# Kernel optimization log

Measured on AMD Instinct MI355X. Metric: run time of the kernel, lower is better.

The kernel has to match this reference:

```python
import jax, jax.numpy as jnp
import numpy as np

CONFIDENCE = 0.1
EPS = 1e-3  # keras BatchNormalization default epsilon
B, H, W, C = 4, 64, 64, 256


def setup_inputs() -> dict:
    key = jax.random.key(0)
    ks = jax.random.split(key, 6)
    return {
        "x": jax.random.normal(ks[0], (B, H, W, C), jnp.float32),
        "ca_gamma": jnp.ones((C,), jnp.float32),
        "ca_beta": jnp.zeros((C,), jnp.float32),
        "ca_mean": jnp.zeros((C,), jnp.float32),
        "ca_var": jnp.ones((C,), jnp.float32),
        "wq": jax.random.normal(ks[1], (C, C), jnp.float32) * 0.05,
        "wk": jax.random.normal(ks[2], (C, C), jnp.float32) * 0.05,
        "wv": jax.random.normal(ks[3], (C, C), jnp.float32) * 0.05,
        "wp": jax.random.normal(ks[4], (C, C), jnp.float32) * 0.05,
        "bn_gamma": jnp.ones((C,), jnp.float32),
        "bn_beta": jnp.zeros((C,), jnp.float32),
        "bn_mean": jnp.zeros((C,), jnp.float32),
        "bn_var": jnp.ones((C,), jnp.float32),
        "w_qkv": jax.random.normal(ks[5], (C, 3), jnp.float32) * 0.05,
    }


def _bn(x, g, b, m, v):
    # keras BatchNormalization, inference mode
    return (x - m) * jax.lax.rsqrt(v + EPS) * g + b


def reference(x, ca_gamma, ca_beta, ca_mean, ca_var, wq, wk, wv, wp,
              bn_gamma, bn_beta, bn_mean, bn_var, w_qkv):
    b, h, w, c = x.shape
    # ---- ChannelAttention (TRACER Channel_Tracer; dropout = identity at inference) ----
    gap = x.mean(axis=(1, 2))                         # [B, C] global average pool
    gn = _bn(gap, ca_gamma, ca_beta, ca_mean, ca_var)  # [B, C]
    q = gn @ wq                                        # 1x1 conv on 1x1 map == matmul
    k = gn @ wk
    v = gn @ wv
    logits = q[:, :, None] * k[:, None, :]             # [B, C, C], head_dim = 1
    score = jax.nn.softmax(logits, axis=-1)
    att = jnp.einsum('bij,bj->bi', score, v)           # [B, C]
    cmask = jax.nn.sigmoid(att @ wp)                   # [B, C] channel mask (alpha)
    ca_out = x * cmask[:, None, None, :] + x           # residual channel re-weighting
    # ---- UnionAttention spatial part ----
    co = _bn(ca_out, bn_gamma, bn_beta, bn_mean, bn_var)
    thr = jnp.percentile(cmask, CONFIDENCE * 100.0, axis=-1,
                         keepdims=True, method='linear')  # [B, 1]
    pmask = jnp.where(cmask > thr, cmask, 0.0)          # percentile masking
    co = co * pmask[:, None, None, :]
    qkv = jnp.einsum('bhwc,cf->bhwf', co, w_qkv)        # [B, H, W, 3] fused q/k/v 1x1 conv
    n = h * w
    qs = qkv[..., 0].reshape(b, n)                      # [B, N], head_dim = 1
    ks_ = qkv[..., 1].reshape(b, n)
    vs = qkv[..., 2].reshape(b, n)
    sl = qs[:, :, None] * ks_[:, None, :]               # [B, N, N] scores (outer product)
    sw = jax.nn.softmax(sl, axis=-1)
    sa = jnp.einsum('bij,bj->bi', sw, vs)               # [B, N]
    return qkv[..., 2:3] + sa.reshape(b, h, w, 1)       # v + attention, [B, H, W, 1]
```

## Files before the change

### kernel.cpp

```cpp
#include <hip/hip_runtime.h>

#define EPS 1e-3f

#define OFF_PGAP   0
#define OFF_A      65536
#define OFF_BIAS   66560
#define OFF_QS     66576
#define OFF_KS     82960
#define OFF_VS     99344

__global__ __launch_bounds__(256) void k_gap(const float* __restrict__ x,
                                             float* __restrict__ pgap) {
    int blk = blockIdx.x;
    int t = threadIdx.x;
    const float* xp = x + (size_t)blk * (64 * 256) + t;
    float s = 0.f;
    #pragma unroll 16
    for (int p = 0; p < 64; ++p) s += xp[(size_t)p * 256];
    pgap[blk * 256 + t] = s;
}

__global__ __launch_bounds__(512) void k_mid(
    const float* __restrict__ pgap,
    const float* __restrict__ cag, const float* __restrict__ cab,
    const float* __restrict__ cam, const float* __restrict__ cav,
    const float* __restrict__ wq, const float* __restrict__ wk,
    const float* __restrict__ wv, const float* __restrict__ wp,
    const float* __restrict__ bng, const float* __restrict__ bnb,
    const float* __restrict__ bnm, const float* __restrict__ bnv,
    const float* __restrict__ wqkv,
    float* __restrict__ Aout, float* __restrict__ biasOut)
{
    __shared__ float gn[256];
    __shared__ float sq[256], sk[256], sv[256], att[256], cm[256], Bc[256];
    __shared__ float red[6144];
    __shared__ float swqkv[768];
    __shared__ float t25, t26, thr;

    int b = blockIdx.x;
    int t = threadIdx.x;
    int cg = t & 63;
    int rg = t >> 6;
    int c4 = cg * 4;

    if (t < 384) {
        swqkv[t] = wqkv[t];
        swqkv[t + 384] = wqkv[t + 384];
    }

    {
        const float* pg = pgap + (size_t)(b * 64 + rg * 8) * 256 + c4;
        float4 s = make_float4(0.f, 0.f, 0.f, 0.f);
        #pragma unroll
        for (int u = 0; u < 8; ++u) {
            float4 v = *(const float4*)(pg + (size_t)u * 256);
            s.x += v.x; s.y += v.y; s.z += v.z; s.w += v.w;
        }
        *(float4*)(red + rg * 256 + c4) = s;
    }
    __syncthreads();
    if (t < 256) {
        float g = 0.f;
        #pragma unroll
        for (int r = 0; r < 8; ++r) g += red[r * 256 + t];
        g *= (1.0f / 4096.0f);
        float sc = cag[t] * rsqrtf(cav[t] + EPS);
        gn[t] = g * sc + (cab[t] - cam[t] * sc);
    }
    __syncthreads();

    {
        int rbase = rg * 32;
        float4 aq = make_float4(0.f, 0.f, 0.f, 0.f);
        float4 ak = aq, av = aq;
        const float* wqp = wq + (size_t)rbase * 256 + c4;
        const float* wkp = wk + (size_t)rbase * 256 + c4;
        const float* wvp = wv + (size_t)rbase * 256 + c4;
        #pragma unroll 8
        for (int i = 0; i < 32; ++i) {
            float g = gn[rbase + i];
            float4 w = *(const float4*)(wqp + (size_t)i * 256);
            aq.x = fmaf(g, w.x, aq.x); aq.y = fmaf(g, w.y, aq.y);
            aq.z = fmaf(g, w.z, aq.z); aq.w = fmaf(g, w.w, aq.w);
        }
        #pragma unroll 8
        for (int i = 0; i < 32; ++i) {
            float g = gn[rbase + i];
            float4 w = *(const float4*)(wkp + (size_t)i * 256);
            ak.x = fmaf(g, w.x, ak.x); ak.y = fmaf(g, w.y, ak.y);
            ak.z = fmaf(g, w.z, ak.z); ak.w = fmaf(g, w.w, ak.w);
        }
        #pragma unroll 8
        for (int i = 0; i < 32; ++i) {
            float g = gn[rbase + i];
            float4 w = *(const float4*)(wvp + (size_t)i * 256);
            av.x = fmaf(g, w.x, av.x); av.y = fmaf(g, w.y, av.y);
            av.z = fmaf(g, w.z, av.z); av.w = fmaf(g, w.w, av.w);
        }
        *(float4*)(red + (0 * 8 + rg) * 256 + c4) = aq;
        *(float4*)(red + (1 * 8 + rg) * 256 + c4) = ak;
        *(float4*)(red + (2 * 8 + rg) * 256 + c4) = av;
    }
    __syncthreads();
    {
        int m = t >> 8, c = t & 255;
        float s = 0.f;
        #pragma unroll
        for (int r = 0; r < 8; ++r) s += red[(m * 8 + r) * 256 + c];
        if (m == 0) sq[c] = s; else sk[c] = s;
        if (t < 256) {
            float s2 = 0.f;
            #pragma unroll
            for (int r = 0; r < 8; ++r) s2 += red[(2 * 8 + r) * 256 + t];
            sv[t] = s2;
        }
    }
    __syncthreads();

    {
        int h = t >> 8, c = t & 255;
        float a = sq[c];
        int jb = h * 128;
        float mx = -1e30f;
        #pragma unroll 8
        for (int j = 0; j < 128; ++j) mx = fmaxf(mx, a * sk[jb + j]);
        float den = 0.f, num = 0.f;
        #pragma unroll 4
        for (int j = 0; j < 128; ++j) {
            float e = __expf(a * sk[jb + j] - mx);
            den += e; num = fmaf(e, sv[jb + j], num);
        }
        red[h * 256 + c] = mx;
        red[512 + h * 256 + c] = den;
        red[1024 + h * 256 + c] = num;
    }
    __syncthreads();
    if (t < 256) {
        float m0 = red[t], m1 = red[256 + t];
        float M = fmaxf(m0, m1);
        float s0 = __expf(m0 - M), s1 = __expf(m1 - M);
        float den = red[512 + t] * s0 + red[768 + t] * s1;
        float num = red[1024 + t] * s0 + red[1280 + t] * s1;
        att[t] = num / den;
    }
    __syncthreads();

    {
        int rbase = rg * 32;
        float4 ac = make_float4(0.f, 0.f, 0.f, 0.f);
        const float* wpp = wp + (size_t)rbase * 256 + c4;
        #pragma unroll 8
        for (int i = 0; i < 32; ++i) {
            float g = att[rbase + i];
            float4 w = *(const float4*)(wpp + (size_t)i * 256);
            ac.x = fmaf(g, w.x, ac.x); ac.y = fmaf(g, w.y, ac.y);
            ac.z = fmaf(g, w.z, ac.z); ac.w = fmaf(g, w.w, ac.w);
        }
        *(float4*)(red + rg * 256 + c4) = ac;
    }
    __syncthreads();
    if (t < 256) {
        float ac = 0.f;
        #pragma unroll
        for (int r = 0; r < 8; ++r) ac += red[r * 256 + t];
        cm[t] = 1.0f / (1.0f + __expf(-ac));
    }
    __syncthreads();

    if (t < 256) {
        float my = cm[t];
        int rank = 0;
        for (int j = 0; j < 256; ++j) {
            float o = cm[j];
            rank += (o < my) ? 1 : ((o == my && j < t) ? 1 : 0);
        }
        if (rank == 25) t25 = my;
        if (rank == 26) t26 = my;
    }
    __syncthreads();
    if (t == 0) thr = t25 + 0.5f * (t26 - t25);
    __syncthreads();

    if (t < 256) {
        float s2 = bng[t] * rsqrtf(bnv[t] + EPS);
        float o2 = bnb[t] - bnm[t] * s2;
        float cc = cm[t];
        float pm = (cc > thr) ? cc : 0.f;
        Aout[b * 256 + t] = (1.f + cc) * s2 * pm;
        Bc[t] = o2 * pm;
    }
    __syncthreads();
    if (t < 3) {
        float s3 = 0.f;
        for (int ch = 0; ch < 256; ++ch) s3 = fmaf(Bc[ch], swqkv[ch * 3 + t], s3);
        biasOut[b * 3 + t] = s3;
    }
}

__global__ __launch_bounds__(256) void k_qkv(
    const float* __restrict__ x, const float* __restrict__ A,
    const float* __restrict__ wqkv, const float* __restrict__ bias,
    float* __restrict__ qs, float* __restrict__ ks, float* __restrict__ vs)
{
    int lane = threadIdx.x & 63;
    int wid = (blockIdx.x * 256 + threadIdx.x) >> 6;
    float4 wA = *(const float4*)(wqkv + 12 * lane);
    float4 wB = *(const float4*)(wqkv + 12 * lane + 4);
    float4 wC = *(const float4*)(wqkv + 12 * lane + 8);
    float w00 = wA.x, w01 = wA.y, w02 = wA.z;
    float w10 = wA.w, w11 = wB.x, w12 = wB.y;
    float w20 = wB.z, w21 = wB.w, w22 = wC.x;
    float w30 = wC.y, w31 = wC.z, w32 = wC.w;
    #pragma unroll
    for (int b = 0; b < 4; ++b) {
        int pix = b * 4096 + wid;
        float4 xv = *(const float4*)(x + (size_t)pix * 256 + 4 * lane);
        float4 A4 = *(const float4*)(A + b * 256 + 4 * lane);
        float t0 = xv.x * A4.x, t1 = xv.y * A4.y;
        float t2 = xv.z * A4.z, t3 = xv.w * A4.w;
        float q = t0 * w00 + t1 * w10 + t2 * w20 + t3 * w30;
        float k = t0 * w01 + t1 * w11 + t2 * w21 + t3 * w31;
        float v = t0 * w02 + t1 * w12 + t2 * w22 + t3 * w32;
        #pragma unroll
        for (int m = 1; m < 64; m <<= 1) {
            q += __shfl_xor(q, m, 64);
            k += __shfl_xor(k, m, 64);
            v += __shfl_xor(v, m, 64);
        }
        if (lane == 0) {
            qs[pix] = q + bias[b * 3 + 0];
            ks[pix] = k + bias[b * 3 + 1];
            vs[pix] = v + bias[b * 3 + 2];
        }
    }
}

__global__ __launch_bounds__(512) void k_attn2(
    const float* __restrict__ qs, const float* __restrict__ ks, const float* __restrict__ vs,
    float* __restrict__ out)
{
    __shared__ float4 skv[2048];
    __shared__ float pden[8][64], pnum[8][64];
    __shared__ float rmax[8], rmin[8];
    int blk = blockIdx.x;
    int b = blk >> 6, ic = blk & 63;
    int t = threadIdx.x;
    int lane = t & 63, sub = t >> 6;
    int base = b * 4096;

    const float4* k4 = (const float4*)(ks + base);
    const float4* v4 = (const float4*)(vs + base);
    float kmx = -1e30f, kmn = 1e30f;
    #pragma unroll
    for (int u = 0; u < 2; ++u) {
        int i = t + u * 512;
        float4 kk = k4[i], vv = v4[i];
        skv[i * 2]     = make_float4(kk.x, vv.x, kk.y, vv.y);
        skv[i * 2 + 1] = make_float4(kk.z, vv.z, kk.w, vv.w);
        kmx = fmaxf(kmx, fmaxf(fmaxf(kk.x, kk.y), fmaxf(kk.z, kk.w)));
        kmn = fminf(kmn, fminf(fminf(kk.x, kk.y), fminf(kk.z, kk.w)));
    }
    #pragma unroll
    for (int m2 = 1; m2 < 64; m2 <<= 1) {
        kmx = fmaxf(kmx, __shfl_xor(kmx, m2, 64));
        kmn = fminf(kmn, __shfl_xor(kmn, m2, 64));
    }
    if (lane == 0) { rmax[sub] = kmx; rmin[sub] = kmn; }
    __syncthreads();
    float mx = rmax[0], mn = rmin[0];
    #pragma unroll
    for (int s = 1; s < 8; ++s) { mx = fmaxf(mx, rmax[s]); mn = fminf(mn, rmin[s]); }

    int row = ic * 64 + lane;
    float a = qs[base + row];
    float m = (a >= 0.f) ? a * mx : a * mn;
    float den0 = 0.f, num0 = 0.f, den1 = 0.f, num1 = 0.f;
    const float4* sp = skv + sub * 256;
    #pragma unroll 4
    for (int j = 0; j < 256; ++j) {
        float4 kv = sp[j];
        float e0 = __expf(fmaf(a, kv.x, -m));
        float e1 = __expf(fmaf(a, kv.z, -m));
        den0 += e0; num0 = fmaf(e0, kv.y, num0);
        den1 += e1; num1 = fmaf(e1, kv.w, num1);
    }
    pden[sub][lane] = den0 + den1;
    pnum[sub][lane] = num0 + num1;
    __syncthreads();
    if (t < 64) {
        float den = 0.f, num = 0.f;
        #pragma unroll
        for (int s = 0; s < 8; ++s) { den += pden[s][t]; num += pnum[s][t]; }
        int r = ic * 64 + t;
        float vrow = (r & 1) ? skv[r >> 1].w : skv[r >> 1].y;
        out[base + r] = vrow + num / den;
    }
}

extern "C" void kernel_launch(void* const* d_in, const int* in_sizes, int n_in,
                              void* d_out, int out_size, void* d_ws, size_t ws_size,
                              hipStream_t stream) {
    const float* x    = (const float*)d_in[0];
    const float* cag  = (const float*)d_in[1];
    const float* cab  = (const float*)d_in[2];
    const float* cam  = (const float*)d_in[3];
    const float* cav  = (const float*)d_in[4];
    const float* wq   = (const float*)d_in[5];
    const float* wk   = (const float*)d_in[6];
    const float* wv   = (const float*)d_in[7];
    const float* wp   = (const float*)d_in[8];
    const float* bng  = (const float*)d_in[9];
    const float* bnb  = (const float*)d_in[10];
    const float* bnm  = (const float*)d_in[11];
    const float* bnv  = (const float*)d_in[12];
    const float* wqkv = (const float*)d_in[13];

    float* ws   = (float*)d_ws;
    float* pgap = ws + OFF_PGAP;
    float* A    = ws + OFF_A;
    float* bias = ws + OFF_BIAS;
    float* qs   = ws + OFF_QS;
    float* ks   = ws + OFF_KS;
    float* vs   = ws + OFF_VS;

    k_gap<<<dim3(256), dim3(256), 0, stream>>>(x, pgap);
    k_mid<<<dim3(4), dim3(512), 0, stream>>>(pgap, cag, cab, cam, cav, wq, wk, wv, wp,
                                             bng, bnb, bnm, bnv, wqkv, A, bias);
    k_qkv<<<dim3(1024), dim3(256), 0, stream>>>(x, A, wqkv, bias, qs, ks, vs);
    k_attn2<<<dim3(256), dim3(512), 0, stream>>>(qs, ks, vs, (float*)d_out);
}
```

Measured before the change: 140.9 us.

## Split channel-attention GEMVs into a parallel kernel and prefetch weights in GAP

Moves the q/k/v GEMV out of the 4-block k_mid kernel into a new 96-block k_qkvmat kernel. Each block handles 8 weight rows for all batches and writes partial sums, which k_mid then reduces. k_gap now uses float4 loads with an in-block reduction, and it also touches the wq/wk/wv/wp weights so they are pulled into cache before the serial stages. The aim is to cut the latency of the low-parallelism middle stage. The cost is an extra kernel launch and a partial-sum buffer round trip.

```diff
diff --git a/kernel.cpp b/kernel.cpp
--- a/kernel.cpp
+++ b/kernel.cpp
@@ -3,37 +3,109 @@
 #define EPS 1e-3f
 
 #define OFF_PGAP   0
-#define OFF_A      65536
-#define OFF_BIAS   66560
-#define OFF_QS     66576
-#define OFF_KS     82960
-#define OFF_VS     99344
+#define OFF_PART   65536
+#define OFF_A      163840
+#define OFF_BIAS   164864
+#define OFF_QS     164880
+#define OFF_KS     181264
+#define OFF_VS     197648
 
 __global__ __launch_bounds__(256) void k_gap(const float* __restrict__ x,
+                                             const float* __restrict__ wq,
+                                             const float* __restrict__ wk,
+                                             const float* __restrict__ wv,
+                                             const float* __restrict__ wp,
                                              float* __restrict__ pgap) {
+    __shared__ float4 red[256];
     int blk = blockIdx.x;
     int t = threadIdx.x;
-    const float* xp = x + (size_t)blk * (64 * 256) + t;
-    float s = 0.f;
-    #pragma unroll 16
-    for (int p = 0; p < 64; ++p) s += xp[(size_t)p * 256];
-    pgap[blk * 256 + t] = s;
-}
-
-__global__ __launch_bounds__(512) void k_mid(
+
+    const float* wmat = (blk < 64) ? wq : (blk < 128) ? wk : (blk < 192) ? wv : wp;
+    float4 wv4 = *(const float4*)(wmat + (size_t)(blk & 63) * 1024 + 4 * t);
+
+    int cg = t & 63;
+    int pg = t >> 6;
+    const float* xp = x + ((size_t)blk * 64 + pg * 16) * 256 + 4 * cg;
+    float4 s = make_float4(0.f, 0.f, 0.f, 0.f);
+    #pragma unroll
+    for (int u = 0; u < 16; ++u) {
+        float4 v = *(const float4*)(xp + (size_t)u * 256);
+        s.x += v.x; s.y += v.y; s.z += v.z; s.w += v.w;
+    }
+    red[pg * 64 + cg] = s;
+    asm volatile("" :: "v"(wv4.x), "v"(wv4.y), "v"(wv4.z), "v"(wv4.w));
+    __syncthreads();
+    if (t < 64) {
+        float4 a = red[t], b4 = red[64 + t], c4 = red[128 + t], d4 = red[192 + t];
+        float4 o = make_float4(a.x + b4.x + c4.x + d4.x,
+                               a.y + b4.y + c4.y + d4.y,
+                               a.z + b4.z + c4.z + d4.z,
+                               a.w + b4.w + c4.w + d4.w);
+        *(float4*)(pgap + blk * 256 + 4 * t) = o;
+    }
+}
+
+__global__ __launch_bounds__(256) void k_qkvmat(
     const float* __restrict__ pgap,
     const float* __restrict__ cag, const float* __restrict__ cab,
     const float* __restrict__ cam, const float* __restrict__ cav,
     const float* __restrict__ wq, const float* __restrict__ wk,
-    const float* __restrict__ wv, const float* __restrict__ wp,
+    const float* __restrict__ wv,
+    float* __restrict__ part)
+{
+    __shared__ float gpart[4][8][4];
+    __shared__ float gn_s[4][8];
+    int blk = blockIdx.x;
+    int m = blk >> 5;
+    int g = blk & 31;
+    int r0 = g * 8;
+    int t = threadIdx.x;
+    const float* W = (m == 0) ? wq : (m == 1) ? wk : wv;
+
+    if (t < 128) {
+        int b = t >> 5, row = (t >> 2) & 7, p = t & 3;
+        const float* pgp = pgap + ((size_t)(b * 64 + p * 16)) * 256 + r0 + row;
+        float s = 0.f;
+        #pragma unroll
+        for (int ch = 0; ch < 16; ++ch) s += pgp[(size_t)ch * 256];
+        gpart[b][row][p] = s;
+    }
+    __syncthreads();
+    if (t < 32) {
+        int b = t >> 3, row = t & 7;
+        float gsum = gpart[b][row][0] + gpart[b][row][1]
+                   + gpart[b][row][2] + gpart[b][row][3];
+        float gv = gsum * (1.0f / 4096.0f);
+        int c = r0 + row;
+        float sc = cag[c] * rsqrtf(cav[c] + EPS);
+        gn_s[b][row] = gv * sc + (cab[c] - cam[c] * sc);
+    }
+    __syncthreads();
+
+    float a0 = 0.f, a1 = 0.f, a2 = 0.f, a3 = 0.f;
+    const float* wp_ = W + (size_t)r0 * 256 + t;
+    #pragma unroll
+    for (int row = 0; row < 8; ++row) {
+        float w = wp_[(size_t)row * 256];
+        a0 = fmaf(gn_s[0][row], w, a0);
+        a1 = fmaf(gn_s[1][row], w, a1);
+        a2 = fmaf(gn_s[2][row], w, a2);
+        a3 = fmaf(gn_s[3][row], w, a3);
+    }
+    float* o = part + (size_t)(m * 32 + g) * 1024 + t;
+    o[0] = a0; o[256] = a1; o[512] = a2; o[768] = a3;
+}
+
+__global__ __launch_bounds__(512) void k_mid(
+    const float* __restrict__ part,
+    const float* __restrict__ wp,
     const float* __restrict__ bng, const float* __restrict__ bnb,
     const float* __restrict__ bnm, const float* __restrict__ bnv,
     const float* __restrict__ wqkv,
     float* __restrict__ Aout, float* __restrict__ biasOut)
 {
-    __shared__ float gn[256];
     __shared__ float sq[256], sk[256], sv[256], att[256], cm[256], Bc[256];
-    __shared__ float red[6144];
+    __shared__ float red[2048];
     __shared__ float swqkv[768];
     __shared__ float t25, t26, thr;
 
@@ -49,69 +121,17 @@
     }
 
     {
-        const float* pg = pgap + (size_t)(b * 64 + rg * 8) * 256 + c4;
-        float4 s = make_float4(0.f, 0.f, 0.f, 0.f);
-        #pragma unroll
-        for (int u = 0; u < 8; ++u) {
-            float4 v = *(const float4*)(pg + (size_t)u * 256);
-            s.x += v.x; s.y += v.y; s.z += v.z; s.w += v.w;
-        }
-        *(float4*)(red + rg * 256 + c4) = s;
-    }
-    __syncthreads();
-    if (t < 256) {
-        float g = 0.f;
-        #pragma unroll
-        for (int r = 0; r < 8; ++r) g += red[r * 256 + t];
-        g *= (1.0f / 4096.0f);
-        float sc = cag[t] * rsqrtf(cav[t] + EPS);
-        gn[t] = g * sc + (cab[t] - cam[t] * sc);
-    }
-    __syncthreads();
-
-    {
-        int rbase = rg * 32;
-        float4 aq = make_float4(0.f, 0.f, 0.f, 0.f);
-        float4 ak = aq, av = aq;
-        const float* wqp = wq + (size_t)rbase * 256 + c4;
-        const float* wkp = wk + (size_t)rbase * 256 + c4;
-        const float* wvp = wv + (size_t)rbase * 256 + c4;
-        #pragma unroll 8
-        for (int i = 0; i < 32; ++i) {
-            float g = gn[rbase + i];
-            float4 w = *(const float4*)(wqp + (size_t)i * 256);
-            aq.x = fmaf(g, w.x, aq.x); aq.y = fmaf(g, w.y, aq.y);
-            aq.z = fmaf(g, w.z, aq.z); aq.w = fmaf(g, w.w, aq.w);
-        }
-        #pragma unroll 8
-        for (int i = 0; i < 32; ++i) {
-            float g = gn[rbase + i];
-            float4 w = *(const float4*)(wkp + (size_t)i * 256);
-            ak.x = fmaf(g, w.x, ak.x); ak.y = fmaf(g, w.y, ak.y);
-            ak.z = fmaf(g, w.z, ak.z); ak.w = fmaf(g, w.w, ak.w);
-        }
-        #pragma unroll 8
-        for (int i = 0; i < 32; ++i) {
-            float g = gn[rbase + i];
-            float4 w = *(const float4*)(wvp + (size_t)i * 256);
-            av.x = fmaf(g, w.x, av.x); av.y = fmaf(g, w.y, av.y);
-            av.z = fmaf(g, w.z, av.z); av.w = fmaf(g, w.w, av.w);
-        }
-        *(float4*)(red + (0 * 8 + rg) * 256 + c4) = aq;
-        *(float4*)(red + (1 * 8 + rg) * 256 + c4) = ak;
-        *(float4*)(red + (2 * 8 + rg) * 256 + c4) = av;
-    }
-    __syncthreads();
-    {
         int m = t >> 8, c = t & 255;
+        const float* p = part + (size_t)m * 32768 + b * 256 + c;
         float s = 0.f;
         #pragma unroll
-        for (int r = 0; r < 8; ++r) s += red[(m * 8 + r) * 256 + c];
+        for (int g2 = 0; g2 < 32; ++g2) s += p[(size_t)g2 * 1024];
         if (m == 0) sq[c] = s; else sk[c] = s;
         if (t < 256) {
+            const float* p2 = part + (size_t)2 * 32768 + b * 256 + t;
             float s2 = 0.f;
             #pragma unroll
-            for (int r = 0; r < 8; ++r) s2 += red[(2 * 8 + r) * 256 + t];
+            for (int g2 = 0; g2 < 32; ++g2) s2 += p2[(size_t)g2 * 1024];
             sv[t] = s2;
         }
     }
@@ -317,15 +337,18 @@
 
     float* ws   = (float*)d_ws;
     float* pgap = ws + OFF_PGAP;
+    float* part = ws + OFF_PART;
     float* A    = ws + OFF_A;
     float* bias = ws + OFF_BIAS;
     float* qs   = ws + OFF_QS;
     float* ks   = ws + OFF_KS;
     float* vs   = ws + OFF_VS;
 
-    k_gap<<<dim3(256), dim3(256), 0, stream>>>(x, pgap);
-    k_mid<<<dim3(4), dim3(512), 0, stream>>>(pgap, cag, cab, cam, cav, wq, wk, wv, wp,
-                                             bng, bnb, bnm, bnv, wqkv, A, bias);
+    k_gap<<<dim3(256), dim3(256), 0, stream>>>(x, wq, wk, wv, wp, pgap);
+    k_qkvmat<<<dim3(96), dim3(256), 0, stream>>>(pgap, cag, cab, cam, cav,
+                                                 wq, wk, wv, part);
+    k_mid<<<dim3(4), dim3(512), 0, stream>>>(part, wp, bng, bnb, bnm, bnv, wqkv,
+                                             A, bias);
     k_qkv<<<dim3(1024), dim3(256), 0, stream>>>(x, A, wqkv, bias, qs, ks, vs);
     k_attn2<<<dim3(256), dim3(512), 0, stream>>>(qs, ks, vs, (float*)d_out);
 }
```

Measured after the change: 137.0 us. -2.8%, faster.

## Fuse four kernels into one persistent kernel with software grid barriers

Applied to the files above, without the earlier changes.

Replaces the four separate launches (GAP, channel-attention mid, qkv projection, spatial attention) with a single 256-block kernel that uses an atomic-counter grid barrier between phases. Before the first barrier each block also touches the weight matrices and BN parameters to warm the cache. Each block loads its share of x for the qkv phase into registers before the mid phase, so those loads overlap with the 4-block serial section. The aim is to remove launch gaps and idle time around the tiny mid kernel. The cost is that correctness depends on all 256 blocks being resident at once, and the barrier spin loop has a timeout fallback.

```diff
diff --git a/kernel.cpp b/kernel.cpp
--- a/kernel.cpp
+++ b/kernel.cpp
@@ -9,19 +9,28 @@
 #define OFF_KS     82960
 #define OFF_VS     99344
 
-__global__ __launch_bounds__(256) void k_gap(const float* __restrict__ x,
-                                             float* __restrict__ pgap) {
-    int blk = blockIdx.x;
-    int t = threadIdx.x;
-    const float* xp = x + (size_t)blk * (64 * 256) + t;
-    float s = 0.f;
-    #pragma unroll 16
-    for (int p = 0; p < 64; ++p) s += xp[(size_t)p * 256];
-    pgap[blk * 256 + t] = s;
+__device__ unsigned g_bar = 0u;
+
+__device__ __forceinline__ void gridbar() {
+    __syncthreads();
+    if (threadIdx.x == 0) {
+        __threadfence();
+        unsigned v = __hip_atomic_fetch_add(&g_bar, 1u, __ATOMIC_RELEASE,
+                                            __HIP_MEMORY_SCOPE_AGENT);
+        unsigned target = (v & ~255u) + 256u;
+        unsigned tries = 0;
+        while (__hip_atomic_load(&g_bar, __ATOMIC_ACQUIRE,
+                                 __HIP_MEMORY_SCOPE_AGENT) < target) {
+            __builtin_amdgcn_s_sleep(1);
+            if (++tries > 20000000u) break;
+        }
+        __threadfence();
+    }
+    __syncthreads();
 }
 
-__global__ __launch_bounds__(512) void k_mid(
-    const float* __restrict__ pgap,
+__global__ __launch_bounds__(512) void mega(
+    const float* __restrict__ x,
     const float* __restrict__ cag, const float* __restrict__ cab,
     const float* __restrict__ cam, const float* __restrict__ cav,
     const float* __restrict__ wq, const float* __restrict__ wk,
@@ -29,271 +38,326 @@
     const float* __restrict__ bng, const float* __restrict__ bnb,
     const float* __restrict__ bnm, const float* __restrict__ bnv,
     const float* __restrict__ wqkv,
-    float* __restrict__ Aout, float* __restrict__ biasOut)
+    float* __restrict__ ws, float* __restrict__ out)
 {
-    __shared__ float gn[256];
-    __shared__ float sq[256], sk[256], sv[256], att[256], cm[256], Bc[256];
-    __shared__ float red[6144];
-    __shared__ float swqkv[768];
-    __shared__ float t25, t26, thr;
-
-    int b = blockIdx.x;
-    int t = threadIdx.x;
-    int cg = t & 63;
-    int rg = t >> 6;
-    int c4 = cg * 4;
-
-    if (t < 384) {
-        swqkv[t] = wqkv[t];
-        swqkv[t + 384] = wqkv[t + 384];
-    }
-
-    {
-        const float* pg = pgap + (size_t)(b * 64 + rg * 8) * 256 + c4;
-        float4 s = make_float4(0.f, 0.f, 0.f, 0.f);
-        #pragma unroll
-        for (int u = 0; u < 8; ++u) {
-            float4 v = *(const float4*)(pg + (size_t)u * 256);
-            s.x += v.x; s.y += v.y; s.z += v.z; s.w += v.w;
-        }
-        *(float4*)(red + rg * 256 + c4) = s;
-    }
-    __syncthreads();
-    if (t < 256) {
-        float g = 0.f;
-        #pragma unroll
-        for (int r = 0; r < 8; ++r) g += red[r * 256 + t];
-        g *= (1.0f / 4096.0f);
-        float sc = cag[t] * rsqrtf(cav[t] + EPS);
-        gn[t] = g * sc + (cab[t] - cam[t] * sc);
-    }
-    __syncthreads();
-
-    {
-        int rbase = rg * 32;
-        float4 aq = make_float4(0.f, 0.f, 0.f, 0.f);
-        float4 ak = aq, av = aq;
-        const float* wqp = wq + (size_t)rbase * 256 + c4;
-        const float* wkp = wk + (size_t)rbase * 256 + c4;
-        const float* wvp = wv + (size_t)rbase * 256 + c4;
-        #pragma unroll 8
-        for (int i = 0; i < 32; ++i) {
-            float g = gn[rbase + i];
-            float4 w = *(const float4*)(wqp + (size_t)i * 256);
-            aq.x = fmaf(g, w.x, aq.x); aq.y = fmaf(g, w.y, aq.y);
-            aq.z = fmaf(g, w.z, aq.z); aq.w = fmaf(g, w.w, aq.w);
-        }
-        #pragma unroll 8
-        for (int i = 0; i < 32; ++i) {
-            float g = gn[rbase + i];
-            float4 w = *(const float4*)(wkp + (size_t)i * 256);
-            ak.x = fmaf(g, w.x, ak.x); ak.y = fmaf(g, w.y, ak.y);
-            ak.z = fmaf(g, w.z, ak.z); ak.w = fmaf(g, w.w, ak.w);
-        }
-        #pragma unroll 8
-        for (int i = 0; i < 32; ++i) {
-            float g = gn[rbase + i];
-            float4 w = *(const float4*)(wvp + (size_t)i * 256);
-            av.x = fmaf(g, w.x, av.x); av.y = fmaf(g, w.y, av.y);
-            av.z = fmaf(g, w.z, av.z); av.w = fmaf(g, w.w, av.w);
-        }
-        *(float4*)(red + (0 * 8 + rg) * 256 + c4) = aq;
-        *(float4*)(red + (1 * 8 + rg) * 256 + c4) = ak;
-        *(float4*)(red + (2 * 8 + rg) * 256 + c4) = av;
-    }
-    __syncthreads();
-    {
-        int m = t >> 8, c = t & 255;
-        float s = 0.f;
-        #pragma unroll
-        for (int r = 0; r < 8; ++r) s += red[(m * 8 + r) * 256 + c];
-        if (m == 0) sq[c] = s; else sk[c] = s;
-        if (t < 256) {
-            float s2 = 0.f;
-            #pragma unroll
-            for (int r = 0; r < 8; ++r) s2 += red[(2 * 8 + r) * 256 + t];
-            sv[t] = s2;
-        }
-    }
-    __syncthreads();
-
-    {
-        int h = t >> 8, c = t & 255;
-        float a = sq[c];
-        int jb = h * 128;
-        float mx = -1e30f;
-        #pragma unroll 8
-        for (int j = 0; j < 128; ++j) mx = fmaxf(mx, a * sk[jb + j]);
-        float den = 0.f, num = 0.f;
-        #pragma unroll 4
-        for (int j = 0; j < 128; ++j) {
-            float e = __expf(a * sk[jb + j] - mx);
-            den += e; num = fmaf(e, sv[jb + j], num);
-        }
-        red[h * 256 + c] = mx;
-        red[512 + h * 256 + c] = den;
-        red[1024 + h * 256 + c] = num;
-    }
-    __syncthreads();
-    if (t < 256) {
-        float m0 = red[t], m1 = red[256 + t];
-        float M = fmaxf(m0, m1);
-        float s0 = __expf(m0 - M), s1 = __expf(m1 - M);
-        float den = red[512 + t] * s0 + red[768 + t] * s1;
-        float num = red[1024 + t] * s0 + red[1280 + t] * s1;
-        att[t] = num / den;
-    }
-    __syncthreads();
-
-    {
-        int rbase = rg * 32;
-        float4 ac = make_float4(0.f, 0.f, 0.f, 0.f);
-        const float* wpp = wp + (size_t)rbase * 256 + c4;
-        #pragma unroll 8
-        for (int i = 0; i < 32; ++i) {
-            float g = att[rbase + i];
-            float4 w = *(const float4*)(wpp + (size_t)i * 256);
-            ac.x = fmaf(g, w.x, ac.x); ac.y = fmaf(g, w.y, ac.y);
-            ac.z = fmaf(g, w.z, ac.z); ac.w = fmaf(g, w.w, ac.w);
-        }
-        *(float4*)(red + rg * 256 + c4) = ac;
-    }
-    __syncthreads();
-    if (t < 256) {
-        float ac = 0.f;
-        #pragma unroll
-        for (int r = 0; r < 8; ++r) ac += red[r * 256 + t];
-        cm[t] = 1.0f / (1.0f + __expf(-ac));
-    }
-    __syncthreads();
-
-    if (t < 256) {
-        float my = cm[t];
-        int rank = 0;
-        for (int j = 0; j < 256; ++j) {
-            float o = cm[j];
-            rank += (o < my) ? 1 : ((o == my && j < t) ? 1 : 0);
-        }
-        if (rank == 25) t25 = my;
-        if (rank == 26) t26 = my;
-    }
-    __syncthreads();
-    if (t == 0) thr = t25 + 0.5f * (t26 - t25);
-    __syncthreads();
-
-    if (t < 256) {
-        float s2 = bng[t] * rsqrtf(bnv[t] + EPS);
-        float o2 = bnb[t] - bnm[t] * s2;
-        float cc = cm[t];
-        float pm = (cc > thr) ? cc : 0.f;
-        Aout[b * 256 + t] = (1.f + cc) * s2 * pm;
-        Bc[t] = o2 * pm;
-    }
-    __syncthreads();
-    if (t < 3) {
-        float s3 = 0.f;
-        for (int ch = 0; ch < 256; ++ch) s3 = fmaf(Bc[ch], swqkv[ch * 3 + t], s3);
-        biasOut[b * 3 + t] = s3;
-    }
-}
-
-__global__ __launch_bounds__(256) void k_qkv(
-    const float* __restrict__ x, const float* __restrict__ A,
-    const float* __restrict__ wqkv, const float* __restrict__ bias,
-    float* __restrict__ qs, float* __restrict__ ks, float* __restrict__ vs)
-{
-    int lane = threadIdx.x & 63;
-    int wid = (blockIdx.x * 256 + threadIdx.x) >> 6;
-    float4 wA = *(const float4*)(wqkv + 12 * lane);
-    float4 wB = *(const float4*)(wqkv + 12 * lane + 4);
-    float4 wC = *(const float4*)(wqkv + 12 * lane + 8);
-    float w00 = wA.x, w01 = wA.y, w02 = wA.z;
-    float w10 = wA.w, w11 = wB.x, w12 = wB.y;
-    float w20 = wB.z, w21 = wB.w, w22 = wC.x;
-    float w30 = wC.y, w31 = wC.z, w32 = wC.w;
-    #pragma unroll
-    for (int b = 0; b < 4; ++b) {
-        int pix = b * 4096 + wid;
-        float4 xv = *(const float4*)(x + (size_t)pix * 256 + 4 * lane);
-        float4 A4 = *(const float4*)(A + b * 256 + 4 * lane);
-        float t0 = xv.x * A4.x, t1 = xv.y * A4.y;
-        float t2 = xv.z * A4.z, t3 = xv.w * A4.w;
-        float q = t0 * w00 + t1 * w10 + t2 * w20 + t3 * w30;
-        float k = t0 * w01 + t1 * w11 + t2 * w21 + t3 * w31;
-        float v = t0 * w02 + t1 * w12 + t2 * w22 + t3 * w32;
-        #pragma unroll
-        for (int m = 1; m < 64; m <<= 1) {
-            q += __shfl_xor(q, m, 64);
-            k += __shfl_xor(k, m, 64);
-            v += __shfl_xor(v, m, 64);
-        }
-        if (lane == 0) {
-            qs[pix] = q + bias[b * 3 + 0];
-            ks[pix] = k + bias[b * 3 + 1];
-            vs[pix] = v + bias[b * 3 + 2];
-        }
-    }
-}
-
-__global__ __launch_bounds__(512) void k_attn2(
-    const float* __restrict__ qs, const float* __restrict__ ks, const float* __restrict__ vs,
-    float* __restrict__ out)
-{
-    __shared__ float4 skv[2048];
-    __shared__ float pden[8][64], pnum[8][64];
-    __shared__ float rmax[8], rmin[8];
+    __shared__ float4 s4[2048];
+    __shared__ float  sA[6144];
+    __shared__ float  sB[2576];
+
+    float* pgap = ws + OFF_PGAP;
+    float* Aw   = ws + OFF_A;
+    float* bias = ws + OFF_BIAS;
+    float* qs   = ws + OFF_QS;
+    float* ks   = ws + OFF_KS;
+    float* vs   = ws + OFF_VS;
+
     int blk = blockIdx.x;
-    int b = blk >> 6, ic = blk & 63;
     int t = threadIdx.x;
     int lane = t & 63, sub = t >> 6;
-    int base = b * 4096;
-
-    const float4* k4 = (const float4*)(ks + base);
-    const float4* v4 = (const float4*)(vs + base);
-    float kmx = -1e30f, kmn = 1e30f;
+
+    {
+        if (t < 256) {
+            const float* wmat = (blk < 64) ? wq : (blk < 128) ? wk
+                              : (blk < 192) ? wv : wp;
+            float4 w4 = *(const float4*)(wmat + (size_t)(blk & 63) * 1024 + 4 * t);
+            asm volatile("" :: "v"(w4.x), "v"(w4.y), "v"(w4.z), "v"(w4.w));
+        }
+        if (blk == 1 && t < 256) {
+            float z = bng[t] + bnb[t] + bnm[t] + bnv[t];
+            asm volatile("" :: "v"(z));
+        }
+        if (blk == 2 && t < 256) {
+            float z = cag[t] + cab[t] + cam[t] + cav[t];
+            asm volatile("" :: "v"(z));
+        }
+        const float* xp = x + ((size_t)blk * 64 + sub * 8) * 256 + 4 * lane;
+        float4 s = make_float4(0.f, 0.f, 0.f, 0.f);
+        #pragma unroll
+        for (int u = 0; u < 8; ++u) {
+            float4 v = *(const float4*)(xp + (size_t)u * 256);
+            s.x += v.x; s.y += v.y; s.z += v.z; s.w += v.w;
+        }
+        s4[sub * 64 + lane] = s;
+        __syncthreads();
+        if (t < 64) {
+            float4 o = s4[t];
+            #pragma unroll
+            for (int p = 1; p < 8; ++p) {
+                float4 v = s4[p * 64 + t];
+                o.x += v.x; o.y += v.y; o.z += v.z; o.w += v.w;
+            }
+            *(float4*)(pgap + blk * 256 + 4 * t) = o;
+        }
+    }
+    gridbar();
+
+    float4 px[2][4];
     #pragma unroll
-    for (int u = 0; u < 2; ++u) {
-        int i = t + u * 512;
-        float4 kk = k4[i], vv = v4[i];
-        skv[i * 2]     = make_float4(kk.x, vv.x, kk.y, vv.y);
-        skv[i * 2 + 1] = make_float4(kk.z, vv.z, kk.w, vv.w);
-        kmx = fmaxf(kmx, fmaxf(fmaxf(kk.x, kk.y), fmaxf(kk.z, kk.w)));
-        kmn = fminf(kmn, fminf(fminf(kk.x, kk.y), fminf(kk.z, kk.w)));
-    }
-    #pragma unroll
-    for (int m2 = 1; m2 < 64; m2 <<= 1) {
-        kmx = fmaxf(kmx, __shfl_xor(kmx, m2, 64));
-        kmn = fminf(kmn, __shfl_xor(kmn, m2, 64));
-    }
-    if (lane == 0) { rmax[sub] = kmx; rmin[sub] = kmn; }
-    __syncthreads();
-    float mx = rmax[0], mn = rmin[0];
-    #pragma unroll
-    for (int s = 1; s < 8; ++s) { mx = fmaxf(mx, rmax[s]); mn = fminf(mn, rmin[s]); }
-
-    int row = ic * 64 + lane;
-    float a = qs[base + row];
-    float m = (a >= 0.f) ? a * mx : a * mn;
-    float den0 = 0.f, num0 = 0.f, den1 = 0.f, num1 = 0.f;
-    const float4* sp = skv + sub * 256;
-    #pragma unroll 4
-    for (int j = 0; j < 256; ++j) {
-        float4 kv = sp[j];
-        float e0 = __expf(fmaf(a, kv.x, -m));
-        float e1 = __expf(fmaf(a, kv.z, -m));
-        den0 += e0; num0 = fmaf(e0, kv.y, num0);
-        den1 += e1; num1 = fmaf(e1, kv.w, num1);
-    }
-    pden[sub][lane] = den0 + den1;
-    pnum[sub][lane] = num0 + num1;
-    __syncthreads();
-    if (t < 64) {
-        float den = 0.f, num = 0.f;
-        #pragma unroll
-        for (int s = 0; s < 8; ++s) { den += pden[s][t]; num += pnum[s][t]; }
-        int r = ic * 64 + t;
-        float vrow = (r & 1) ? skv[r >> 1].w : skv[r >> 1].y;
-        out[base + r] = vrow + num / den;
+    for (int j = 0; j < 2; ++j)
+        #pragma unroll
+        for (int bb = 0; bb < 4; ++bb)
+            px[j][bb] = *(const float4*)(
+                x + (size_t)(bb * 4096 + blk * 8 + sub + j * 2048) * 256 + 4 * lane);
+    float4 wAv = *(const float4*)(wqkv + 12 * lane);
+    float4 wBv = *(const float4*)(wqkv + 12 * lane + 4);
+    float4 wCv = *(const float4*)(wqkv + 12 * lane + 8);
+
+    if (blk < 4) {
+        int b = blk;
+        int c4 = lane * 4;
+        int rg = sub;
+        float* gn  = sB;
+        float* sq  = sB + 256;
+        float* sk  = sB + 512;
+        float* sv  = sB + 768;
+        float* att = sB + 1024;
+        float* cm  = sB + 1280;
+        float* Bc  = sB + 1536;
+        float* swq = sB + 1792;
+        float* red = sA;
+
+        if (t < 384) { swq[t] = wqkv[t]; swq[t + 384] = wqkv[t + 384]; }
+
+        {
+            const float* pg = pgap + (size_t)(b * 64 + rg * 8) * 256 + c4;
+            float4 s = make_float4(0.f, 0.f, 0.f, 0.f);
+            #pragma unroll
+            for (int u = 0; u < 8; ++u) {
+                float4 v = *(const float4*)(pg + (size_t)u * 256);
+                s.x += v.x; s.y += v.y; s.z += v.z; s.w += v.w;
+            }
+            *(float4*)(red + rg * 256 + c4) = s;
+        }
+        __syncthreads();
+        if (t < 256) {
+            float g = 0.f;
+            #pragma unroll
+            for (int r = 0; r < 8; ++r) g += red[r * 256 + t];
+            g *= (1.0f / 4096.0f);
+            float sc = cag[t] * rsqrtf(cav[t] + EPS);
+            gn[t] = g * sc + (cab[t] - cam[t] * sc);
+        }
+        __syncthreads();
+
+        {
+            int rbase = rg * 32;
+            float4 aq = make_float4(0.f, 0.f, 0.f, 0.f);
+            float4 ak = aq, av = aq;
+            const float* wqp = wq + (size_t)rbase * 256 + c4;
+            const float* wkp = wk + (size_t)rbase * 256 + c4;
+            const float* wvp = wv + (size_t)rbase * 256 + c4;
+            #pragma unroll 8
+            for (int i = 0; i < 32; ++i) {
+                float g = gn[rbase + i];
+                float4 w = *(const float4*)(wqp + (size_t)i * 256);
+                aq.x = fmaf(g, w.x, aq.x); aq.y = fmaf(g, w.y, aq.y);
+                aq.z = fmaf(g, w.z, aq.z); aq.w = fmaf(g, w.w, aq.w);
+            }
+            #pragma unroll 8
+            for (int i = 0; i < 32; ++i) {
+                float g = gn[rbase + i];
+                float4 w = *(const float4*)(wkp + (size_t)i * 256);
+                ak.x = fmaf(g, w.x, ak.x); ak.y = fmaf(g, w.y, ak.y);
+                ak.z = fmaf(g, w.z, ak.z); ak.w = fmaf(g, w.w, ak.w);
+            }
+            #pragma unroll 8
+            for (int i = 0; i < 32; ++i) {
+                float g = gn[rbase + i];
+                float4 w = *(const float4*)(wvp + (size_t)i * 256);
+                av.x = fmaf(g, w.x, av.x); av.y = fmaf(g, w.y, av.y);
+                av.z = fmaf(g, w.z, av.z); av.w = fmaf(g, w.w, av.w);
+            }
+            *(float4*)(red + (0 * 8 + rg) * 256 + c4) = aq;
+            *(float4*)(red + (1 * 8 + rg) * 256 + c4) = ak;
+            *(float4*)(red + (2 * 8 + rg) * 256 + c4) = av;
+        }
+        __syncthreads();
+        {
+            int m2 = t >> 8, c = t & 255;
+            float s = 0.f;
+            #pragma unroll
+            for (int r = 0; r < 8; ++r) s += red[(m2 * 8 + r) * 256 + c];
+            if (m2 == 0) sq[c] = s; else sk[c] = s;
+            if (t < 256) {
+                float s2 = 0.f;
+                #pragma unroll
+                for (int r = 0; r < 8; ++r) s2 += red[(16 + r) * 256 + t];
+                sv[t] = s2;
+            }
+        }
+        __syncthreads();
+
+        {
+            int h = t >> 8, c = t & 255;
+            float a = sq[c];
+            int jb = h * 128;
+            float mx = -1e30f;
+            #pragma unroll 8
+            for (int j = 0; j < 128; ++j) mx = fmaxf(mx, a * sk[jb + j]);
+            float den = 0.f, num = 0.f;
+            #pragma unroll 4
+            for (int j = 0; j < 128; ++j) {
+                float e = __expf(a * sk[jb + j] - mx);
+                den += e; num = fmaf(e, sv[jb + j], num);
+            }
+            red[h * 256 + c] = mx;
+            red[512 + h * 256 + c] = den;
+            red[1024 + h * 256 + c] = num;
+        }
+        __syncthreads();
+        if (t < 256) {
+            float m0 = red[t], m1 = red[256 + t];
+            float M = fmaxf(m0, m1);
+            float s0 = __expf(m0 - M), s1 = __expf(m1 - M);
+            float den = red[512 + t] * s0 + red[768 + t] * s1;
+            float num = red[1024 + t] * s0 + red[1280 + t] * s1;
+            att[t] = num / den;
+        }
+        __syncthreads();
+
+        {
+            int rbase = rg * 32;
+            float4 ac = make_float4(0.f, 0.f, 0.f, 0.f);
+            const float* wpp = wp + (size_t)rbase * 256 + c4;
+            #pragma unroll 8
+            for (int i = 0; i < 32; ++i) {
+                float g = att[rbase + i];
+                float4 w = *(const float4*)(wpp + (size_t)i * 256);
+                ac.x = fmaf(g, w.x, ac.x); ac.y = fmaf(g, w.y, ac.y);
+                ac.z = fmaf(g, w.z, ac.z); ac.w = fmaf(g, w.w, ac.w);
+            }
+            *(float4*)(red + rg * 256 + c4) = ac;
+        }
+        __syncthreads();
+        if (t < 256) {
+            float ac = 0.f;
+            #pragma unroll
+            for (int r = 0; r < 8; ++r) ac += red[r * 256 + t];
+            cm[t] = 1.0f / (1.0f + __expf(-ac));
+        }
+        __syncthreads();
+
+        if (t < 256) {
+            float my = cm[t];
+            int rank = 0;
+            for (int j = 0; j < 256; ++j) {
+                float o = cm[j];
+                rank += (o < my) ? 1 : ((o == my && j < t) ? 1 : 0);
+            }
+            if (rank == 25) sB[2560] = my;
+            if (rank == 26) sB[2561] = my;
+        }
+        __syncthreads();
+        if (t == 0) sB[2562] = sB[2560] + 0.5f * (sB[2561] - sB[2560]);
+        __syncthreads();
+
+        if (t < 256) {
+            float s2 = bng[t] * rsqrtf(bnv[t] + EPS);
+            float o2 = bnb[t] - bnm[t] * s2;
+            float cc = cm[t];
+            float thr = sB[2562];
+            float pm = (cc > thr) ? cc : 0.f;
+            Aw[b * 256 + t] = (1.f + cc) * s2 * pm;
+            Bc[t] = o2 * pm;
+        }
+        __syncthreads();
+        if (t < 3) {
+            float s3 = 0.f;
+            for (int ch = 0; ch < 256; ++ch) s3 = fmaf(Bc[ch], swq[ch * 3 + t], s3);
+            bias[b * 3 + t] = s3;
+        }
+    }
+    gridbar();
+
+    {
+        float w00 = wAv.x, w01 = wAv.y, w02 = wAv.z;
+        float w10 = wAv.w, w11 = wBv.x, w12 = wBv.y;
+        float w20 = wBv.z, w21 = wBv.w, w22 = wCv.x;
+        float w30 = wCv.y, w31 = wCv.z, w32 = wCv.w;
+        int wid = blk * 8 + sub;
+        #pragma unroll
+        for (int bb = 0; bb < 4; ++bb) {
+            float4 A4 = *(const float4*)(Aw + bb * 256 + 4 * lane);
+            float bq = bias[bb * 3 + 0];
+            float bk = bias[bb * 3 + 1];
+            float bv = bias[bb * 3 + 2];
+            #pragma unroll
+            for (int j = 0; j < 2; ++j) {
+                int pix = bb * 4096 + wid + j * 2048;
+                float4 xv = px[j][bb];
+                float t0 = xv.x * A4.x, t1 = xv.y * A4.y;
+                float t2 = xv.z * A4.z, t3 = xv.w * A4.w;
+                float q = t0 * w00 + t1 * w10 + t2 * w20 + t3 * w30;
+                float k = t0 * w01 + t1 * w11 + t2 * w21 + t3 * w31;
+                float v = t0 * w02 + t1 * w12 + t2 * w22 + t3 * w32;
+                #pragma unroll
+                for (int m2 = 1; m2 < 64; m2 <<= 1) {
+                    q += __shfl_xor(q, m2, 64);
+                    k += __shfl_xor(k, m2, 64);
+                    v += __shfl_xor(v, m2, 64);
+                }
+                if (lane == 0) {
+                    qs[pix] = q + bq; ks[pix] = k + bk; vs[pix] = v + bv;
+                }
+            }
+        }
+    }
+    gridbar();
+
+    {
+        float* pden = sA;
+        float* pnum = sA + 512;
+        float* rmax = sB;
+        float* rmin = sB + 8;
+        int b = blk >> 6, ic = blk & 63;
+        int base = b * 4096;
+        const float4* k4 = (const float4*)(ks + base);
+        const float4* v4 = (const float4*)(vs + base);
+        float kmx = -1e30f, kmn = 1e30f;
+        #pragma unroll
+        for (int u = 0; u < 2; ++u) {
+            int i = t + u * 512;
+            float4 kk = k4[i], vv = v4[i];
+            s4[i * 2]     = make_float4(kk.x, vv.x, kk.y, vv.y);
+            s4[i * 2 + 1] = make_float4(kk.z, vv.z, kk.w, vv.w);
+            kmx = fmaxf(kmx, fmaxf(fmaxf(kk.x, kk.y), fmaxf(kk.z, kk.w)));
+            kmn = fminf(kmn, fminf(fminf(kk.x, kk.y), fminf(kk.z, kk.w)));
+        }
+        #pragma unroll
+        for (int m2 = 1; m2 < 64; m2 <<= 1) {
+            kmx = fmaxf(kmx, __shfl_xor(kmx, m2, 64));
+            kmn = fminf(kmn, __shfl_xor(kmn, m2, 64));
+        }
+        if (lane == 0) { rmax[sub] = kmx; rmin[sub] = kmn; }
+        __syncthreads();
+        float mx = rmax[0], mn = rmin[0];
+        #pragma unroll
+        for (int s = 1; s < 8; ++s) { mx = fmaxf(mx, rmax[s]); mn = fminf(mn, rmin[s]); }
+
+        int row = ic * 64 + lane;
+        float a = qs[base + row];
+        float m = (a >= 0.f) ? a * mx : a * mn;
+        float den0 = 0.f, num0 = 0.f, den1 = 0.f, num1 = 0.f;
+        const float4* sp = s4 + sub * 256;
+        #pragma unroll 4
+        for (int j = 0; j < 256; ++j) {
+            float4 kv = sp[j];
+            float e0 = __expf(fmaf(a, kv.x, -m));
+            float e1 = __expf(fmaf(a, kv.z, -m));
+            den0 += e0; num0 = fmaf(e0, kv.y, num0);
+            den1 += e1; num1 = fmaf(e1, kv.w, num1);
+        }
+        pden[sub * 64 + lane] = den0 + den1;
+        pnum[sub * 64 + lane] = num0 + num1;
+        __syncthreads();
+        if (t < 64) {
+            float den = 0.f, num = 0.f;
+            #pragma unroll
+            for (int s = 0; s < 8; ++s) { den += pden[s * 64 + t]; num += pnum[s * 64 + t]; }
+            int r = ic * 64 + t;
+            float vrow = (r & 1) ? s4[r >> 1].w : s4[r >> 1].y;
+            out[base + r] = vrow + num / den;
+        }
     }
 }
 
@@ -315,17 +379,9 @@
     const float* bnv  = (const float*)d_in[12];
     const float* wqkv = (const float*)d_in[13];
 
-    float* ws   = (float*)d_ws;
-    float* pgap = ws + OFF_PGAP;
-    float* A    = ws + OFF_A;
-    float* bias = ws + OFF_BIAS;
-    float* qs   = ws + OFF_QS;
-    float* ks   = ws + OFF_KS;
-    float* vs   = ws + OFF_VS;
-
-    k_gap<<<dim3(256), dim3(256), 0, stream>>>(x, pgap);
-    k_mid<<<dim3(4), dim3(512), 0, stream>>>(pgap, cag, cab, cam, cav, wq, wk, wv, wp,
-                                             bng, bnb, bnm, bnv, wqkv, A, bias);
-    k_qkv<<<dim3(1024), dim3(256), 0, stream>>>(x, A, wqkv, bias, qs, ks, vs);
-    k_attn2<<<dim3(256), dim3(512), 0, stream>>>(qs, ks, vs, (float*)d_out);
+    float* ws = (float*)d_ws;
+    mega<<<dim3(256), dim3(512), 0, stream>>>(x, cag, cab, cam, cav,
+                                              wq, wk, wv, wp,
+                                              bng, bnb, bnm, bnv, wqkv,
+                                              ws, (float*)d_out);
 }
```

Result: slower. 279.1 us (+98.1%).
